# Performance work log

Measured on AMD Instinct MI355X. Metric: run time of the kernel, lower is better.

The kernel has to match this reference:

```python
import jax, jax.numpy as jnp
import numpy as np

QLEN, BSZ, D_MODEL = 1024, 4, 1024
N_HEAD, D_HEAD = 16, 64
RLEN = QLEN  # rlen == klen -> classic _rel_shift path
LN_EPS = 1e-5


def setup_inputs() -> dict:
    key = jax.random.key(0)
    ks = jax.random.split(key, 9)
    s = 0.02
    w = jax.random.normal(ks[0], (QLEN, BSZ, D_MODEL), jnp.float32)
    r = jax.random.normal(ks[1], (RLEN, D_MODEL), jnp.float32)
    # causal mask: True = masked (future positions)
    attn_mask = jnp.triu(jnp.ones((QLEN, QLEN), jnp.bool_), k=1)
    qkv_w = jax.random.normal(ks[2], (D_MODEL, 3 * N_HEAD * D_HEAD), jnp.float32) * s
    r_w = jax.random.normal(ks[3], (D_MODEL, N_HEAD * D_HEAD), jnp.float32) * s
    o_w = jax.random.normal(ks[4], (N_HEAD * D_HEAD, D_MODEL), jnp.float32) * s
    r_r_bias = jax.random.normal(ks[5], (N_HEAD, D_HEAD), jnp.float32) * s
    r_w_bias = jax.random.normal(ks[6], (N_HEAD, D_HEAD), jnp.float32) * s
    ln_g = jnp.ones((D_MODEL,), jnp.float32)
    ln_b = jnp.zeros((D_MODEL,), jnp.float32)
    return {"w": w, "r": r, "attn_mask": attn_mask, "qkv_w": qkv_w,
            "r_w": r_w, "o_w": o_w, "r_r_bias": r_r_bias,
            "r_w_bias": r_w_bias, "ln_g": ln_g, "ln_b": ln_b}


def _rel_shift(x):
    # x: [qlen, klen, bsz, n_head] -> Transformer-XL relative shift
    q, k, b, n = x.shape
    zero_pad = jnp.zeros((q, 1, b, n), x.dtype)
    x_padded = jnp.concatenate([zero_pad, x], axis=1)      # [q, k+1, b, n]
    x_padded = x_padded.reshape(k + 1, q, b, n)
    return x_padded[1:].reshape(q, k, b, n)


def _layer_norm(x, g, b):
    mu = jnp.mean(x, axis=-1, keepdims=True)
    var = jnp.mean(jnp.square(x - mu), axis=-1, keepdims=True)
    return (x - mu) * jax.lax.rsqrt(var + LN_EPS) * g + b


def reference(w, r, attn_mask, qkv_w, r_w, o_w, r_r_bias, r_w_bias, ln_g, ln_b):
    qlen, bsz, _ = w.shape
    H, D = r_r_bias.shape
    scale = 1.0 / D ** 0.5

    w_heads = w @ qkv_w                                    # [q, b, 3*H*D]
    q_h, k_h, v_h = jnp.split(w_heads, 3, axis=-1)
    q_h = q_h.reshape(qlen, bsz, H, D)
    k_h = k_h.reshape(qlen, bsz, H, D)
    v_h = v_h.reshape(qlen, bsz, H, D)
    r_k = (r @ r_w).reshape(-1, H, D)                      # [rlen, H, D]

    AC = jnp.einsum('ibnd,jbnd->ijbn', q_h + r_w_bias, k_h)
    BD = _rel_shift(jnp.einsum('ibnd,jnd->ijbn', q_h + r_r_bias, r_k))
    score = (AC + BD) * scale                              # [q, k, b, n]
    score = jnp.where(attn_mask[:, :, None, None], -1e30, score)

    prob = jax.nn.softmax(score, axis=1)
    vec = jnp.einsum('ijbn,jbnd->ibnd', prob, v_h).reshape(qlen, bsz, H * D)
    attn_out = vec @ o_w
    return _layer_norm(w + attn_out, ln_g, ln_b)
```

## Files before the change

kernel.cpp:

```cpp
#include <hip/hip_runtime.h>
#include <hip/hip_bf16.h>

#define SEQ    1024
#define BSZW   4
#define DMODEL 1024
#define NHEAD  16
#define DHEAD  64
#define MROWS  (SEQ*BSZW)
#define QKVN   (3*NHEAD*DHEAD)

typedef __attribute__((ext_vector_type(8))) short short8;
typedef __attribute__((ext_vector_type(4))) float f32x4;

__device__ __forceinline__ float bf2f(short s) {
    union { int i; float f; } u; u.i = ((int)(unsigned short)s) << 16; return u.f;
}
__device__ __forceinline__ short f2bf(float f) {
    union { float f; unsigned int u; } v; v.f = f;
    unsigned int r = v.u + 0x7FFFu + ((v.u >> 16) & 1u);
    return (short)(unsigned short)(r >> 16);
}

__device__ __forceinline__ void async16(const void* g, void* s) {
    __builtin_amdgcn_global_load_lds(
        (__attribute__((address_space(1))) void*)(g),
        (__attribute__((address_space(3))) void*)(s), 16, 0, 0);
}

__global__ __launch_bounds__(256) void conv_all(const float* __restrict__ w,
                                                const float* __restrict__ r,
                                                short* __restrict__ Wb,
                                                short* __restrict__ rb)
{
    int bx = blockIdx.x;
    const float* in; short* out; int idx;
    if (bx < 4096) { in = w; out = Wb; idx = (bx * 256 + threadIdx.x) * 4; }
    else           { in = r; out = rb; idx = ((bx - 4096) * 256 + threadIdx.x) * 4; }
    float4 v = *(const float4*)(in + idx);
    out[idx + 0] = f2bf(v.x);
    out[idx + 1] = f2bf(v.y);
    out[idx + 2] = f2bf(v.z);
    out[idx + 3] = f2bf(v.w);
}

__global__ __launch_bounds__(256) void trans_all(const float* __restrict__ qkv_w,
                                                 const float* __restrict__ r_w,
                                                 const float* __restrict__ o_w,
                                                 short* __restrict__ QKVt,
                                                 short* __restrict__ RWt,
                                                 short* __restrict__ OWt)
{
    const int z = blockIdx.z;
    const int bx = blockIdx.x, by = blockIdx.y;
    const float* in; short* out; int C;
    if (z == 0)      { in = qkv_w; out = QKVt; C = QKVN; }
    else if (z == 1) { in = r_w;   out = RWt;  C = DMODEL; if (bx >= 32) return; }
    else             { in = o_w;   out = OWt;  C = DMODEL; if (bx >= 32) return; }
    const int R = DMODEL;
    __shared__ short t[32][33];
    const int tid = threadIdx.x;
    const int r = tid >> 5, c = tid & 31;
    #pragma unroll
    for (int rr = 0; rr < 4; ++rr) {
        int rl = r + rr * 8;
        t[c][rl] = f2bf(in[(size_t)(by * 32 + rl) * C + bx * 32 + c]);
    }
    __syncthreads();
    #pragma unroll
    for (int rr = 0; rr < 4; ++rr) {
        int rl = r + rr * 8;
        out[(size_t)(bx * 32 + rl) * R + by * 32 + c] = t[rl][c];
    }
}

__global__ __launch_bounds__(256) void vtrans(const short* __restrict__ in,
                                              short* __restrict__ out)
{
    __shared__ short t[32][33];
    const int tid = threadIdx.x;
    const int r = tid >> 5, c = tid & 31;
    const int bx = blockIdx.x, by = blockIdx.y, bh = blockIdx.z;
    #pragma unroll
    for (int rr = 0; rr < 4; ++rr) {
        int rl = r + rr * 8;
        t[c][rl] = in[((size_t)bh * SEQ + bx * 32 + rl) * DHEAD + by * 32 + c];
    }
    __syncthreads();
    #pragma unroll
    for (int rr = 0; rr < 4; ++rr) {
        int rl = r + rr * 8;
        out[((size_t)bh * DHEAD + by * 32 + rl) * SEQ + bx * 32 + c] = t[rl][c];
    }
}

#define GEMM_BODY_128(A_, Bt_, K_)                                             \
    __shared__ short As[128 * 32];                                              \
    __shared__ short Bs[128 * 32];                                              \
    const int w = tid >> 6, lane = tid & 63;                                    \
    const int L15 = lane & 15, quad = lane >> 4;                                \
    const int mq = (w & 1) * 64, nq = (w >> 1) * 64;                            \
    f32x4 acc[4][4];                                                            \
    _Pragma("unroll")                                                           \
    for (int i = 0; i < 4; ++i)                                                 \
        _Pragma("unroll")                                                       \
        for (int j = 0; j < 4; ++j) acc[i][j] = (f32x4){0.f, 0.f, 0.f, 0.f};    \
    const int srow  = w * 16 + (lane >> 2);                                     \
    const int schnk = ((lane & 3) ^ (lane >> 4)) * 8;                           \
    const int rpA = (quad ^ (L15 >> 2)) * 8;                                    \
    for (int k0 = 0; k0 < K_; k0 += 32) {                                       \
        __syncthreads();                                                        \
        _Pragma("unroll")                                                       \
        for (int q = 0; q < 2; ++q) {                                           \
            async16(A_ + (size_t)(m0 + q * 64 + srow) * K_ + k0 + schnk,        \
                    &As[(q * 64 + w * 16) * 32]);                               \
            async16(Bt_ + (size_t)(n0 + q * 64 + srow) * K_ + k0 + schnk,       \
                    &Bs[(q * 64 + w * 16) * 32]);                               \
        }                                                                       \
        __syncthreads();                                                        \
        short8 a[4], b[4];                                                      \
        _Pragma("unroll")                                                       \
        for (int rt = 0; rt < 4; ++rt)                                          \
            a[rt] = *(const short8*)&As[(mq + rt * 16 + L15) * 32 + rpA];       \
        _Pragma("unroll")                                                       \
        for (int ct = 0; ct < 4; ++ct)                                          \
            b[ct] = *(const short8*)&Bs[(nq + ct * 16 + L15) * 32 + rpA];       \
        _Pragma("unroll")                                                       \
        for (int rt = 0; rt < 4; ++rt)                                          \
            _Pragma("unroll")                                                   \
            for (int ct = 0; ct < 4; ++ct)                                      \
                acc[rt][ct] = __builtin_amdgcn_mfma_f32_16x16x32_bf16(          \
                    a[rt], b[ct], acc[rt][ct], 0, 0, 0);                        \
    }

__global__ __launch_bounds__(256) void qkv_rk_mfma(const short* __restrict__ Wb,
                                                   const short* __restrict__ QKVt,
                                                   const short* __restrict__ rbuf,
                                                   const short* __restrict__ RWt,
                                                   const float* __restrict__ rwb,
                                                   const float* __restrict__ rrb,
                                                   short* __restrict__ Qwb,
                                                   short* __restrict__ Qrb,
                                                   short* __restrict__ Kb,
                                                   short* __restrict__ Vb,
                                                   short* __restrict__ RK)
{
    const int tid = threadIdx.x;
    const int by = blockIdx.y;
    const bool isrk = (by >= 32);
    if (isrk && blockIdx.x >= 8) return;
    const short* A_  = isrk ? rbuf : Wb;
    const short* Bt_ = isrk ? RWt : QKVt;
    const int m0 = (isrk ? (by - 32) : by) * 128;
    const int n0 = blockIdx.x * 128;
    GEMM_BODY_128(A_, Bt_, 1024)

    if (isrk) {
        const int h = (n0 + nq) >> 6;
        #pragma unroll
        for (int rt = 0; rt < 4; ++rt)
            #pragma unroll
            for (int g = 0; g < 4; ++g) {
                int m = m0 + mq + rt * 16 + quad * 4 + g;
                #pragma unroll
                for (int ct = 0; ct < 4; ++ct)
                    RK[((size_t)h * SEQ + m) * DHEAD + ct * 16 + L15] =
                        f2bf(acc[rt][ct][g]);
            }
        return;
    }
    const int nb = n0 + nq;
    const int chunk = nb >> 10;
    const int h = (nb >> 6) & 15;
    float rw4[4], rr4[4];
    if (chunk == 0) {
        #pragma unroll
        for (int ct = 0; ct < 4; ++ct) {
            rw4[ct] = rwb[h * DHEAD + ct * 16 + L15];
            rr4[ct] = rrb[h * DHEAD + ct * 16 + L15];
        }
    }
    #pragma unroll
    for (int rt = 0; rt < 4; ++rt)
        #pragma unroll
        for (int g = 0; g < 4; ++g) {
            int m = m0 + mq + rt * 16 + quad * 4 + g;
            int qi = m >> 2, b = m & 3;
            size_t rowbase = ((size_t)(b * NHEAD + h) * SEQ + qi) * DHEAD;
            #pragma unroll
            for (int ct = 0; ct < 4; ++ct) {
                int d = ct * 16 + L15;
                float v = acc[rt][ct][g];
                if (chunk == 0) {
                    Qwb[rowbase + d] = f2bf(v + rw4[ct]);
                    Qrb[rowbase + d] = f2bf(v + rr4[ct]);
                } else if (chunk == 1) {
                    Kb[rowbase + d] = f2bf(v);
                } else {
                    Vb[rowbase + d] = f2bf(v);
                }
            }
        }
}

__global__ __launch_bounds__(256) void oproj_mfma(const short* __restrict__ A,
                                                  const short* __restrict__ Bt,
                                                  float* __restrict__ C)
{
    __shared__ short As[128 * 32];
    __shared__ short Bs[64 * 32];
    const int tid = threadIdx.x;
    const int w = tid >> 6, lane = tid & 63;
    const int L15 = lane & 15, quad = lane >> 4;
    const int n0 = blockIdx.x * 64, m0 = blockIdx.y * 128;
    const int mq = w * 32;
    f32x4 acc[2][4];
    #pragma unroll
    for (int i = 0; i < 2; ++i)
        #pragma unroll
        for (int j = 0; j < 4; ++j) acc[i][j] = (f32x4){0.f, 0.f, 0.f, 0.f};
    const int srow  = w * 16 + (lane >> 2);
    const int schnk = ((lane & 3) ^ (lane >> 4)) * 8;
    const int rpA = (quad ^ (L15 >> 2)) * 8;
    for (int k0 = 0; k0 < 1024; k0 += 32) {
        __syncthreads();
        #pragma unroll
        for (int q = 0; q < 2; ++q)
            async16(A + (size_t)(m0 + q * 64 + srow) * 1024 + k0 + schnk,
                    &As[(q * 64 + w * 16) * 32]);
        async16(Bt + (size_t)(n0 + srow) * 1024 + k0 + schnk, &Bs[(w * 16) * 32]);
        __syncthreads();
        short8 a[2], b[4];
        #pragma unroll
        for (int rt = 0; rt < 2; ++rt)
            a[rt] = *(const short8*)&As[(mq + rt * 16 + L15) * 32 + rpA];
        #pragma unroll
        for (int ct = 0; ct < 4; ++ct)
            b[ct] = *(const short8*)&Bs[(ct * 16 + L15) * 32 + rpA];
        #pragma unroll
        for (int rt = 0; rt < 2; ++rt)
            #pragma unroll
            for (int ct = 0; ct < 4; ++ct)
                acc[rt][ct] = __builtin_amdgcn_mfma_f32_16x16x32_bf16(
                    a[rt], b[ct], acc[rt][ct], 0, 0, 0);
    }
    #pragma unroll
    for (int rt = 0; rt < 2; ++rt)
        #pragma unroll
        for (int g = 0; g < 4; ++g) {
            int m = m0 + mq + rt * 16 + quad * 4 + g;
            #pragma unroll
            for (int ct = 0; ct < 4; ++ct)
                C[(size_t)m * DMODEL + n0 + ct * 16 + L15] = acc[rt][ct][g];
        }
}

__global__ __launch_bounds__(256) void attn_mfma(const short* __restrict__ Qw,
                                                 const short* __restrict__ Qr,
                                                 const short* __restrict__ Kg,
                                                 const short* __restrict__ Vt,
                                                 const short* __restrict__ RK,
                                                 short* __restrict__ ATT)
{
    __shared__ short Ks[2][64 * 64];
    __shared__ short Vts[2][64 * 64];
    __shared__ short Pv[4][16][72];

    const int tid  = threadIdx.x;
    const int w    = tid >> 6;
    const int lane = tid & 63;
    const int L15  = lane & 15;
    const int quad = lane >> 4;
    const int bh   = blockIdx.x;
    const int itA  = blockIdx.y;
    const int itB  = 15 - itA;
    const int h    = bh & (NHEAD - 1);
    const int b    = bh >> 4;
    const int C    = 63 - 16 * w;

    const short* Kbh = Kg + (size_t)bh * SEQ * DHEAD;
    const short* Vbh = Vt + (size_t)bh * DHEAD * SEQ;
    const short* Rh  = RK + (size_t)h * SEQ * DHEAD;

    const int srow  = w * 8 + (lane >> 3);
    const int schnk = ((lane & 7) ^ (lane >> 3)) * 8;
    const int rp0 = ((quad)     ^ (L15 & 7)) * 8;
    const int rp1 = ((quad + 4) ^ (L15 & 7)) * 8;

    int ib[4]; bool selhi[4];
    #pragma unroll
    for (int g = 0; g < 4; ++g) {
        int r = quad * 4 + g;
        ib[g] = (((quad << 4) | ((L15 + 15 - r) & 15)) << 2);
        selhi[g] = (L15 > r);
    }

    int it = itA;
    short8 qwf[2], qrf[2];
    {
        const short* qb = Qw + ((size_t)bh * SEQ + it * 64 + w * 16 + L15) * DHEAD + quad * 8;
        qwf[0] = *(const short8*)qb;
        qwf[1] = *(const short8*)(qb + 32);
        const short* qc = Qr + ((size_t)bh * SEQ + it * 64 + w * 16 + L15) * DHEAD + quad * 8;
        qrf[0] = *(const short8*)qc;
        qrf[1] = *(const short8*)(qc + 32);
    }

    f32x4 O[4];
    float mrow[4], lrow[4];
    #pragma unroll
    for (int c = 0; c < 4; ++c) { O[c] = (f32x4){0.f, 0.f, 0.f, 0.f}; }
    #pragma unroll
    for (int g = 0; g < 4; ++g) { mrow[g] = -1e30f; lrow[g] = 0.f; }

    #pragma unroll
    for (int q = 0; q < 2; ++q) {
        int rr = q * 32 + srow;
        async16(Kbh + (size_t)rr * DHEAD + schnk, &Ks[0][(q * 32 + w * 8) * 64]);
        async16(Vbh + (size_t)rr * SEQ + schnk,   &Vts[0][(q * 32 + w * 8) * 64]);
    }

    for (int k = 0; k < 17; ++k) {
        if (k == itA + 1) {
            #pragma unroll
            for (int g = 0; g < 4; ++g) {
                float inv = 1.0f / lrow[g];
                int i = itA * 64 + w * 16 + quad * 4 + g;
                #pragma unroll
                for (int ct = 0; ct < 4; ++ct)
                    ATT[((size_t)i * BSZW + b) * DMODEL + h * DHEAD + ct * 16 + L15] =
                        f2bf(O[ct][g] * inv);
            }
            it = itB;
            #pragma unroll
            for (int c = 0; c < 4; ++c) O[c] = (f32x4){0.f, 0.f, 0.f, 0.f};
            #pragma unroll
            for (int g = 0; g < 4; ++g) { mrow[g] = -1e30f; lrow[g] = 0.f; }
            const short* qb = Qw + ((size_t)bh * SEQ + it * 64 + w * 16 + L15) * DHEAD + quad * 8;
            qwf[0] = *(const short8*)qb;
            qwf[1] = *(const short8*)(qb + 32);
            const short* qc = Qr + ((size_t)bh * SEQ + it * 64 + w * 16 + L15) * DHEAD + quad * 8;
            qrf[0] = *(const short8*)qc;
            qrf[1] = *(const short8*)(qc + 32);
        }
        const int jt  = (k <= itA) ? k : (k - itA - 1);
        const int buf = k & 1;
        const int j0  = jt * 64;
        const int rel0 = 960 + 64 * (jt - it);

        __syncthreads();

        if (k < 16) {
            const int kn  = k + 1;
            const int jtn = (kn <= itA) ? kn : (kn - itA - 1);
            const int j0n = jtn * 64;
            #pragma unroll
            for (int q = 0; q < 2; ++q) {
                int rr = q * 32 + srow;
                async16(Kbh + (size_t)(j0n + rr) * DHEAD + schnk,
                        &Ks[buf ^ 1][(q * 32 + w * 8) * 64]);
                async16(Vbh + (size_t)rr * SEQ + j0n + schnk,
                        &Vts[buf ^ 1][(q * 32 + w * 8) * 64]);
            }
        }

        short8 rb0[5], rb1[5];
        #pragma unroll
        for (int cp = 0; cp < 5; ++cp) {
            int ct  = (3 - w) + cp;
            int rel = rel0 + ct * 16 + L15;
            rel = (rel > SEQ - 1) ? (SEQ - 1) : rel;
            const short* rp = Rh + (size_t)rel * DHEAD + quad * 8;
            rb0[cp] = *(const short8*)rp;
            rb1[cp] = *(const short8*)(rp + 32);
        }

        f32x4 S[4];
        #pragma unroll
        for (int ct = 0; ct < 4; ++ct) {
            short8 b0 = *(const short8*)&Ks[buf][(ct * 16 + L15) * 64 + rp0];
            short8 b1 = *(const short8*)&Ks[buf][(ct * 16 + L15) * 64 + rp1];
            f32x4 acc = (f32x4){0.f, 0.f, 0.f, 0.f};
            acc = __builtin_amdgcn_mfma_f32_16x16x32_bf16(qwf[0], b0, acc, 0, 0, 0);
            acc = __builtin_amdgcn_mfma_f32_16x16x32_bf16(qwf[1], b1, acc, 0, 0, 0);
            S[ct] = acc;
        }

        f32x4 p[5];
        #pragma unroll
        for (int cp = 0; cp < 5; ++cp) {
            f32x4 pp = (f32x4){0.f, 0.f, 0.f, 0.f};
            pp = __builtin_amdgcn_mfma_f32_16x16x32_bf16(qrf[0], rb0[cp], pp, 0, 0, 0);
            pp = __builtin_amdgcn_mfma_f32_16x16x32_bf16(qrf[1], rb1[cp], pp, 0, 0, 0);
            p[cp] = pp;
        }

        float qq[5][4];
        #pragma unroll
        for (int cp = 0; cp < 5; ++cp)
            #pragma unroll
            for (int g = 0; g < 4; ++g)
                qq[cp][g] = __int_as_float(
                    __builtin_amdgcn_ds_bpermute(ib[g], __float_as_int(p[cp][g])));
        #pragma unroll
        for (int ct = 0; ct < 4; ++ct)
            #pragma unroll
            for (int g = 0; g < 4; ++g) {
                float bd = selhi[g] ? qq[ct + 1][g] : qq[ct][g];
                S[ct][g] = (S[ct][g] + bd) * 0.125f;
            }

        if (jt == it) {
            #pragma unroll
            for (int ct = 0; ct < 4; ++ct)
                #pragma unroll
                for (int g = 0; g < 4; ++g) {
                    int i = it * 64 + w * 16 + quad * 4 + g;
                    int j = j0 + ct * 16 + L15;
                    if (j > i) S[ct][g] = -1e30f;
                }
        }

        float mt[4];
        #pragma unroll
        for (int g = 0; g < 4; ++g)
            mt[g] = fmaxf(fmaxf(S[0][g], S[1][g]), fmaxf(S[2][g], S[3][g]));
        #pragma unroll
        for (int off = 1; off < 16; off <<= 1)
            #pragma unroll
            for (int g = 0; g < 4; ++g)
                mt[g] = fmaxf(mt[g], __shfl_xor(mt[g], off, 64));

        float al[4];
        #pragma unroll
        for (int g = 0; g < 4; ++g) {
            float mn = fmaxf(mrow[g], mt[g]);
            al[g] = __expf(mrow[g] - mn);
            mrow[g] = mn;
        }
        #pragma unroll
        for (int ct = 0; ct < 4; ++ct)
            #pragma unroll
            for (int g = 0; g < 4; ++g)
                S[ct][g] = __expf(S[ct][g] - mrow[g]);

        float rs[4];
        #pragma unroll
        for (int g = 0; g < 4; ++g)
            rs[g] = (S[0][g] + S[1][g]) + (S[2][g] + S[3][g]);
        #pragma unroll
        for (int off = 1; off < 16; off <<= 1)
            #pragma unroll
            for (int g = 0; g < 4; ++g)
                rs[g] += __shfl_xor(rs[g], off, 64);
        #pragma unroll
        for (int g = 0; g < 4; ++g)
            lrow[g] = lrow[g] * al[g] + rs[g];
        #pragma unroll
        for (int ct = 0; ct < 4; ++ct)
            #pragma unroll
            for (int g = 0; g < 4; ++g)
                O[ct][g] *= al[g];

        #pragma unroll
        for (int ct = 0; ct < 4; ++ct)
            #pragma unroll
            for (int g = 0; g < 4; ++g)
                Pv[w][quad * 4 + g][ct * 16 + L15] = f2bf(S[ct][g]);
        short8 pa0 = *(const short8*)&Pv[w][L15][quad * 8];
        short8 pa1 = *(const short8*)&Pv[w][L15][32 + quad * 8];

        #pragma unroll
        for (int ct = 0; ct < 4; ++ct) {
            short8 v0 = *(const short8*)&Vts[buf][(ct * 16 + L15) * 64 + rp0];
            short8 v1 = *(const short8*)&Vts[buf][(ct * 16 + L15) * 64 + rp1];
            O[ct] = __builtin_amdgcn_mfma_f32_16x16x32_bf16(pa0, v0, O[ct], 0, 0, 0);
            O[ct] = __builtin_amdgcn_mfma_f32_16x16x32_bf16(pa1, v1, O[ct], 0, 0, 0);
        }
    }

    #pragma unroll
    for (int g = 0; g < 4; ++g) {
        float inv = 1.0f / lrow[g];
        int i = itB * 64 + w * 16 + quad * 4 + g;
        #pragma unroll
        for (int ct = 0; ct < 4; ++ct)
            ATT[((size_t)i * BSZW + b) * DMODEL + h * DHEAD + ct * 16 + L15] =
                f2bf(O[ct][g] * inv);
    }
}

__global__ __launch_bounds__(256) void ln_kernel(const float* __restrict__ w,
                                                 const float* __restrict__ AO,
                                                 const float* __restrict__ g,
                                                 const float* __restrict__ bb,
                                                 float* __restrict__ out)
{
    __shared__ float red[256];
    __shared__ float sh_mu, sh_rs;
    const int m = blockIdx.x;
    const int tid = threadIdx.x;
    const int j0 = tid * 4;
    float4 xw = *(const float4*)(w + (size_t)m * DMODEL + j0);
    float4 xa = *(const float4*)(AO + (size_t)m * DMODEL + j0);
    float x[4] = {xw.x + xa.x, xw.y + xa.y, xw.z + xa.z, xw.w + xa.w};
    red[tid] = x[0] + x[1] + x[2] + x[3];
    __syncthreads();
    for (int st = 128; st > 0; st >>= 1) {
        if (tid < st) red[tid] += red[tid + st];
        __syncthreads();
    }
    if (tid == 0) sh_mu = red[0] * (1.0f / DMODEL);
    __syncthreads();
    const float mu = sh_mu;
    float v = 0.0f;
    #pragma unroll
    for (int k = 0; k < 4; ++k) { float d = x[k] - mu; v += d * d; }
    red[tid] = v;
    __syncthreads();
    for (int st = 128; st > 0; st >>= 1) {
        if (tid < st) red[tid] += red[tid + st];
        __syncthreads();
    }
    if (tid == 0) sh_rs = rsqrtf(red[0] * (1.0f / DMODEL) + 1e-5f);
    __syncthreads();
    const float rs = sh_rs;
    float4 g4 = *(const float4*)(g + j0);
    float4 b4 = *(const float4*)(bb + j0);
    float4 o4;
    o4.x = (x[0] - mu) * rs * g4.x + b4.x;
    o4.y = (x[1] - mu) * rs * g4.y + b4.y;
    o4.z = (x[2] - mu) * rs * g4.z + b4.z;
    o4.w = (x[3] - mu) * rs * g4.w + b4.w;
    *(float4*)(out + (size_t)m * DMODEL + j0) = o4;
}

extern "C" void kernel_launch(void* const* d_in, const int* in_sizes, int n_in,
                              void* d_out, int out_size, void* d_ws, size_t ws_size,
                              hipStream_t stream)
{
    (void)in_sizes; (void)n_in; (void)out_size; (void)ws_size;
    const float* w     = (const float*)d_in[0];
    const float* r     = (const float*)d_in[1];
    const float* qkv_w = (const float*)d_in[3];
    const float* r_w   = (const float*)d_in[4];
    const float* o_w   = (const float*)d_in[5];
    const float* rrb   = (const float*)d_in[6];
    const float* rwb   = (const float*)d_in[7];
    const float* ln_g  = (const float*)d_in[8];
    const float* ln_b  = (const float*)d_in[9];
    float* out = (float*)d_out;

    const size_t M1 = 1024 * 1024;
    short* Wb   = (short*)d_ws;
    short* QKVt = Wb   + 4 * M1;
    short* rb   = QKVt + 3 * M1;
    short* RWt  = rb   + 1 * M1;
    short* OWt  = RWt  + 1 * M1;
    short* Qwb  = OWt  + 1 * M1;
    short* Qrb  = Qwb  + 4 * M1;
    short* Kb   = Qrb  + 4 * M1;
    short* Vb   = Kb   + 4 * M1;
    short* Vtb  = Vb   + 4 * M1;
    short* RKb  = Vtb  + 4 * M1;
    short* ATTb = Vb;
    float* AO   = (float*)d_ws;

    conv_all<<<5120, 256, 0, stream>>>(w, r, Wb, rb);
    trans_all<<<dim3(QKVN / 32, DMODEL / 32, 3), 256, 0, stream>>>(qkv_w, r_w, o_w,
                                                                   QKVt, RWt, OWt);

    qkv_rk_mfma<<<dim3(QKVN / 128, 40), 256, 0, stream>>>(Wb, QKVt, rb, RWt,
                                                          rwb, rrb,
                                                          Qwb, Qrb, Kb, Vb, RKb);
    vtrans<<<dim3(SEQ / 32, DHEAD / 32, BSZW * NHEAD), 256, 0, stream>>>(Vb, Vtb);
    attn_mfma<<<dim3(BSZW * NHEAD, 8), 256, 0, stream>>>(Qwb, Qrb, Kb, Vtb, RKb, ATTb);
    oproj_mfma<<<dim3(DMODEL / 64, MROWS / 128), 256, 0, stream>>>(ATTb, OWt, AO);
    ln_kernel<<<MROWS, 256, 0, stream>>>(w, AO, ln_g, ln_b, out);
}
```

Baseline: 261.8 us.

## Launch one attention block per query tile and merge prep kernels

The conversion and transpose prep kernels become one launch, using a fourth z-slice for the fp32-to-bf16 conversion of w and r. The attention kernel no longer pairs query tiles itA and 15-itA inside one block; it launches 16 blocks per batch-head, each handling a single causal query tile, with heaviest tiles scheduled first. The relative-shift gather switches from ds_bpermute lane shuffles to writing the positional scores to shared memory as bf16 and reading them back at shifted offsets. This adds parallelism and removes a launch, at the cost of uneven per-block work and an extra bf16 rounding of the positional term.

```diff
diff --git a/kernel.cpp b/kernel.cpp
--- a/kernel.cpp
+++ b/kernel.cpp
@@ -27,30 +27,33 @@
         (__attribute__((address_space(3))) void*)(s), 16, 0, 0);
 }
 
-__global__ __launch_bounds__(256) void conv_all(const float* __restrict__ w,
+__global__ __launch_bounds__(256) void prep_all(const float* __restrict__ w,
                                                 const float* __restrict__ r,
+                                                const float* __restrict__ qkv_w,
+                                                const float* __restrict__ r_w,
+                                                const float* __restrict__ o_w,
                                                 short* __restrict__ Wb,
-                                                short* __restrict__ rb)
-{
-    int bx = blockIdx.x;
-    const float* in; short* out; int idx;
-    if (bx < 4096) { in = w; out = Wb; idx = (bx * 256 + threadIdx.x) * 4; }
-    else           { in = r; out = rb; idx = ((bx - 4096) * 256 + threadIdx.x) * 4; }
-    float4 v = *(const float4*)(in + idx);
-    out[idx + 0] = f2bf(v.x);
-    out[idx + 1] = f2bf(v.y);
-    out[idx + 2] = f2bf(v.z);
-    out[idx + 3] = f2bf(v.w);
-}
-
-__global__ __launch_bounds__(256) void trans_all(const float* __restrict__ qkv_w,
-                                                 const float* __restrict__ r_w,
-                                                 const float* __restrict__ o_w,
-                                                 short* __restrict__ QKVt,
-                                                 short* __restrict__ RWt,
-                                                 short* __restrict__ OWt)
+                                                short* __restrict__ rb,
+                                                short* __restrict__ QKVt,
+                                                short* __restrict__ RWt,
+                                                short* __restrict__ OWt)
 {
     const int z = blockIdx.z;
+    const int tid = threadIdx.x;
+    if (z == 3) {
+        size_t flat = (size_t)blockIdx.y * 96 + blockIdx.x;
+        if (flat >= 2560) return;
+        size_t idx = flat * 2048 + (size_t)tid * 8;
+        const float* in = w; short* out = Wb;
+        if (idx >= (size_t)4194304) { in = r; out = rb; idx -= 4194304; flat = 0; }
+        float4 a = *(const float4*)(in + idx);
+        float4 b = *(const float4*)(in + idx + 4);
+        out[idx + 0] = f2bf(a.x); out[idx + 1] = f2bf(a.y);
+        out[idx + 2] = f2bf(a.z); out[idx + 3] = f2bf(a.w);
+        out[idx + 4] = f2bf(b.x); out[idx + 5] = f2bf(b.y);
+        out[idx + 6] = f2bf(b.z); out[idx + 7] = f2bf(b.w);
+        return;
+    }
     const int bx = blockIdx.x, by = blockIdx.y;
     const float* in; short* out; int C;
     if (z == 0)      { in = qkv_w; out = QKVt; C = QKVN; }
@@ -58,17 +61,16 @@
     else             { in = o_w;   out = OWt;  C = DMODEL; if (bx >= 32) return; }
     const int R = DMODEL;
     __shared__ short t[32][33];
-    const int tid = threadIdx.x;
-    const int r = tid >> 5, c = tid & 31;
+    const int rr0 = tid >> 5, c = tid & 31;
     #pragma unroll
     for (int rr = 0; rr < 4; ++rr) {
-        int rl = r + rr * 8;
+        int rl = rr0 + rr * 8;
         t[c][rl] = f2bf(in[(size_t)(by * 32 + rl) * C + bx * 32 + c]);
     }
     __syncthreads();
     #pragma unroll
     for (int rr = 0; rr < 4; ++rr) {
-        int rl = r + rr * 8;
+        int rl = rr0 + rr * 8;
         out[(size_t)(bx * 32 + rl) * R + by * 32 + c] = t[rl][c];
     }
 }
@@ -263,7 +265,7 @@
 {
     __shared__ short Ks[2][64 * 64];
     __shared__ short Vts[2][64 * 64];
-    __shared__ short Pv[4][16][72];
+    __shared__ short Pbuf[4][16][136];
 
     const int tid  = threadIdx.x;
     const int w    = tid >> 6;
@@ -271,8 +273,7 @@
     const int L15  = lane & 15;
     const int quad = lane >> 4;
     const int bh   = blockIdx.x;
-    const int itA  = blockIdx.y;
-    const int itB  = 15 - itA;
+    const int it   = 15 - (int)blockIdx.y;
     const int h    = bh & (NHEAD - 1);
     const int b    = bh >> 4;
     const int C    = 63 - 16 * w;
@@ -286,15 +287,6 @@
     const int rp0 = ((quad)     ^ (L15 & 7)) * 8;
     const int rp1 = ((quad + 4) ^ (L15 & 7)) * 8;
 
-    int ib[4]; bool selhi[4];
-    #pragma unroll
-    for (int g = 0; g < 4; ++g) {
-        int r = quad * 4 + g;
-        ib[g] = (((quad << 4) | ((L15 + 15 - r) & 15)) << 2);
-        selhi[g] = (L15 > r);
-    }
-
-    int it = itA;
     short8 qwf[2], qrf[2];
     {
         const short* qb = Qw + ((size_t)bh * SEQ + it * 64 + w * 16 + L15) * DHEAD + quad * 8;
@@ -319,40 +311,15 @@
         async16(Vbh + (size_t)rr * SEQ + schnk,   &Vts[0][(q * 32 + w * 8) * 64]);
     }
 
-    for (int k = 0; k < 17; ++k) {
-        if (k == itA + 1) {
-            #pragma unroll
-            for (int g = 0; g < 4; ++g) {
-                float inv = 1.0f / lrow[g];
-                int i = itA * 64 + w * 16 + quad * 4 + g;
-                #pragma unroll
-                for (int ct = 0; ct < 4; ++ct)
-                    ATT[((size_t)i * BSZW + b) * DMODEL + h * DHEAD + ct * 16 + L15] =
-                        f2bf(O[ct][g] * inv);
-            }
-            it = itB;
-            #pragma unroll
-            for (int c = 0; c < 4; ++c) O[c] = (f32x4){0.f, 0.f, 0.f, 0.f};
-            #pragma unroll
-            for (int g = 0; g < 4; ++g) { mrow[g] = -1e30f; lrow[g] = 0.f; }
-            const short* qb = Qw + ((size_t)bh * SEQ + it * 64 + w * 16 + L15) * DHEAD + quad * 8;
-            qwf[0] = *(const short8*)qb;
-            qwf[1] = *(const short8*)(qb + 32);
-            const short* qc = Qr + ((size_t)bh * SEQ + it * 64 + w * 16 + L15) * DHEAD + quad * 8;
-            qrf[0] = *(const short8*)qc;
-            qrf[1] = *(const short8*)(qc + 32);
-        }
-        const int jt  = (k <= itA) ? k : (k - itA - 1);
-        const int buf = k & 1;
+    for (int jt = 0; jt <= it; ++jt) {
+        const int buf = jt & 1;
         const int j0  = jt * 64;
         const int rel0 = 960 + 64 * (jt - it);
 
         __syncthreads();
 
-        if (k < 16) {
-            const int kn  = k + 1;
-            const int jtn = (kn <= itA) ? kn : (kn - itA - 1);
-            const int j0n = jtn * 64;
+        if (jt < it) {
+            const int j0n = j0 + 64;
             #pragma unroll
             for (int q = 0; q < 2; ++q) {
                 int rr = q * 32 + srow;
@@ -385,30 +352,27 @@
             S[ct] = acc;
         }
 
-        f32x4 p[5];
         #pragma unroll
         for (int cp = 0; cp < 5; ++cp) {
-            f32x4 pp = (f32x4){0.f, 0.f, 0.f, 0.f};
-            pp = __builtin_amdgcn_mfma_f32_16x16x32_bf16(qrf[0], rb0[cp], pp, 0, 0, 0);
-            pp = __builtin_amdgcn_mfma_f32_16x16x32_bf16(qrf[1], rb1[cp], pp, 0, 0, 0);
-            p[cp] = pp;
-        }
-
-        float qq[5][4];
-        #pragma unroll
-        for (int cp = 0; cp < 5; ++cp)
+            int ct = (3 - w) + cp;
+            f32x4 p = (f32x4){0.f, 0.f, 0.f, 0.f};
+            p = __builtin_amdgcn_mfma_f32_16x16x32_bf16(qrf[0], rb0[cp], p, 0, 0, 0);
+            p = __builtin_amdgcn_mfma_f32_16x16x32_bf16(qrf[1], rb1[cp], p, 0, 0, 0);
             #pragma unroll
             for (int g = 0; g < 4; ++g)
-                qq[cp][g] = __int_as_float(
-                    __builtin_amdgcn_ds_bpermute(ib[g], __float_as_int(p[cp][g])));
-        #pragma unroll
-        for (int ct = 0; ct < 4; ++ct)
+                Pbuf[w][quad * 4 + g][ct * 16 + L15] = f2bf(p[g]);
+        }
+
+        #pragma unroll
+        for (int ct = 0; ct < 4; ++ct) {
             #pragma unroll
             for (int g = 0; g < 4; ++g) {
-                float bd = selhi[g] ? qq[ct + 1][g] : qq[ct][g];
+                int r = quad * 4 + g;
+                int t = ct * 16 + L15 - r + C;
+                float bd = bf2f(Pbuf[w][r][t]);
                 S[ct][g] = (S[ct][g] + bd) * 0.125f;
             }
-
+        }
         if (jt == it) {
             #pragma unroll
             for (int ct = 0; ct < 4; ++ct)
@@ -465,9 +429,9 @@
         for (int ct = 0; ct < 4; ++ct)
             #pragma unroll
             for (int g = 0; g < 4; ++g)
-                Pv[w][quad * 4 + g][ct * 16 + L15] = f2bf(S[ct][g]);
-        short8 pa0 = *(const short8*)&Pv[w][L15][quad * 8];
-        short8 pa1 = *(const short8*)&Pv[w][L15][32 + quad * 8];
+                Pbuf[w][quad * 4 + g][ct * 16 + L15] = f2bf(S[ct][g]);
+        short8 pa0 = *(const short8*)&Pbuf[w][L15][quad * 8];
+        short8 pa1 = *(const short8*)&Pbuf[w][L15][32 + quad * 8];
 
         #pragma unroll
         for (int ct = 0; ct < 4; ++ct) {
@@ -481,7 +445,7 @@
     #pragma unroll
     for (int g = 0; g < 4; ++g) {
         float inv = 1.0f / lrow[g];
-        int i = itB * 64 + w * 16 + quad * 4 + g;
+        int i = it * 64 + w * 16 + quad * 4 + g;
         #pragma unroll
         for (int ct = 0; ct < 4; ++ct)
             ATT[((size_t)i * BSZW + b) * DMODEL + h * DHEAD + ct * 16 + L15] =
@@ -565,15 +529,14 @@
     short* ATTb = Vb;
     float* AO   = (float*)d_ws;
 
-    conv_all<<<5120, 256, 0, stream>>>(w, r, Wb, rb);
-    trans_all<<<dim3(QKVN / 32, DMODEL / 32, 3), 256, 0, stream>>>(qkv_w, r_w, o_w,
-                                                                   QKVt, RWt, OWt);
+    prep_all<<<dim3(QKVN / 32, DMODEL / 32, 4), 256, 0, stream>>>(
+        w, r, qkv_w, r_w, o_w, Wb, rb, QKVt, RWt, OWt);
 
     qkv_rk_mfma<<<dim3(QKVN / 128, 40), 256, 0, stream>>>(Wb, QKVt, rb, RWt,
                                                           rwb, rrb,
                                                           Qwb, Qrb, Kb, Vb, RKb);
     vtrans<<<dim3(SEQ / 32, DHEAD / 32, BSZW * NHEAD), 256, 0, stream>>>(Vb, Vtb);
-    attn_mfma<<<dim3(BSZW * NHEAD, 8), 256, 0, stream>>>(Qwb, Qrb, Kb, Vtb, RKb, ATTb);
+    attn_mfma<<<dim3(BSZW * NHEAD, 16), 256, 0, stream>>>(Qwb, Qrb, Kb, Vtb, RKb, ATTb);
     oproj_mfma<<<dim3(DMODEL / 64, MROWS / 128), 256, 0, stream>>>(ATTb, OWt, AO);
     ln_kernel<<<MROWS, 256, 0, stream>>>(w, AO, ln_g, ln_b, out);
 }
```

Measured after the change: 248.4 us. 1.05x faster.
